# Kernel tuning notes

Measured on AMD Instinct MI355X. Metric: run time of the kernel, lower is better.

## Reference

```python
import jax, jax.numpy as jnp
import numpy as np

B, T, C = 2, 2048, 1024
N_HEAD = 16
HEAD_DIM = C // N_HEAD


def setup_inputs() -> dict:
    key = jax.random.key(0)
    ks = jax.random.split(key, 5)
    s = 0.02
    return {
        "x": jax.random.normal(ks[0], (B, T, C), dtype=jnp.float32),
        "W_kqv": jax.random.normal(ks[1], (C, 3 * C), dtype=jnp.float32) * s,
        "b_kqv": jax.random.normal(ks[2], (3 * C,), dtype=jnp.float32) * s,
        "W_proj": jax.random.normal(ks[3], (C, C), dtype=jnp.float32) * s,
        "b_proj": jax.random.normal(ks[4], (C,), dtype=jnp.float32) * s,
    }


def reference(x, W_kqv, b_kqv, W_proj, b_proj):
    Bx, Tx, Cx = x.shape
    qkv = x @ W_kqv + b_kqv                      # [B, T, 3C]
    q, k, v = jnp.split(qkv, 3, axis=-1)
    # [B, H, T, D]
    q = q.reshape(Bx, Tx, N_HEAD, HEAD_DIM).transpose(0, 2, 1, 3)
    k = k.reshape(Bx, Tx, N_HEAD, HEAD_DIM).transpose(0, 2, 1, 3)
    v = v.reshape(Bx, Tx, N_HEAD, HEAD_DIM).transpose(0, 2, 1, 3)
    scale = 1.0 / jnp.sqrt(jnp.asarray(HEAD_DIM, dtype=x.dtype))
    att = jnp.einsum("bhqd,bhkd->bhqk", q, k) * scale  # [B, H, T, T]
    causal = jnp.tril(jnp.ones((Tx, Tx), dtype=bool))   # [T, T]
    att = jnp.where(causal[None, None], att, jnp.float32(-jnp.inf))
    att = jax.nn.softmax(att, axis=-1)
    y = jnp.einsum("bhqk,bhkd->bhqd", att, v)            # [B, H, T, D]
    y = y.transpose(0, 2, 1, 3).reshape(Bx, Tx, Cx)
    out = y @ W_proj + b_proj
    return out, k, v
```

## Files before the change

kernel.cpp:

```cpp
#include <hip/hip_runtime.h>


#define DEVI __device__ __forceinline__

typedef unsigned short ushort_t;
typedef unsigned long long u64_t;
typedef __attribute__((ext_vector_type(4))) unsigned short us4;
typedef __attribute__((ext_vector_type(8))) unsigned short ushort8;
typedef __attribute__((ext_vector_type(4))) float f32x4;
typedef __attribute__((ext_vector_type(8))) __bf16 bf16x8;

DEVI unsigned short f2bf(float f) {
  union { float f; unsigned int u; } c; c.f = f;
  unsigned int u = c.u;
  unsigned int r = (u + 0x7FFFu + ((u >> 16) & 1u)) >> 16;
  return (unsigned short)r;
}

DEVI float exp2v(float x) {
  float r;
  asm("v_exp_f32 %0, %1\n\ts_nop 0" : "=v"(r) : "v"(x));
  return r;
}

DEVI unsigned int cvtpk(float lo, float hi) {
  unsigned int r;
  asm("v_cvt_pk_bf16_f32 %0, %1, %2" : "=v"(r) : "v"(lo), "v"(hi));
  return r;
}

DEVI f32x4 mfma16(ushort8 a, ushort8 b, f32x4 c) {
  return __builtin_amdgcn_mfma_f32_16x16x32_bf16(
      __builtin_bit_cast(bf16x8, a), __builtin_bit_cast(bf16x8, b), c, 0, 0, 0);
}

typedef const __attribute__((address_space(1))) void* gptr_t;
typedef __attribute__((address_space(3))) void* lptr_t;
#define GLOAD_LDS16(g, l) \
  __builtin_amdgcn_global_load_lds((gptr_t)(g), (lptr_t)(l), 16, 0, 0)

DEVI void bar() {
  asm volatile("" ::: "memory");
  __builtin_amdgcn_s_barrier();
  asm volatile("" ::: "memory");
}
#define VMCNT(n) asm volatile("s_waitcnt vmcnt(" #n ")" ::: "memory")


__global__ void cast_x_kernel(const float* __restrict__ in,
                              ushort_t* __restrict__ out, int n8) {
  int i = blockIdx.x * blockDim.x + threadIdx.x;
  if (i >= n8) return;
  const f32x4* p = (const f32x4*)in;
  f32x4 a = p[2 * i], b = p[2 * i + 1];
  ushort8 o;
  o[0] = f2bf(a[0]); o[1] = f2bf(a[1]); o[2] = f2bf(a[2]); o[3] = f2bf(a[3]);
  o[4] = f2bf(b[0]); o[5] = f2bf(b[1]); o[6] = f2bf(b[2]); o[7] = f2bf(b[3]);
  ((ushort8*)out)[i] = o;
}

__global__ void transpose_cast_kernel(const float* __restrict__ in,
                                      ushort_t* __restrict__ out, int R, int Cin) {
  __shared__ float tile[32][33];
  int c0 = blockIdx.x * 32, r0 = blockIdx.y * 32;
  int tx = threadIdx.x & 31, ty = threadIdx.x >> 5;
#pragma unroll
  for (int it = 0; it < 4; ++it)
    tile[ty + it * 8][tx] = in[(size_t)(r0 + ty + it * 8) * Cin + c0 + tx];
  __syncthreads();
#pragma unroll
  for (int it = 0; it < 4; ++it)
    out[(size_t)(c0 + ty + it * 8) * R + r0 + tx] = f2bf(tile[tx][ty + it * 8]);
}


__global__ __launch_bounds__(256) void gemm_bt_kernel(
    const ushort_t* __restrict__ A, const ushort_t* __restrict__ Bt,
    const float* __restrict__ bias, float* __restrict__ outF,
    float* __restrict__ outK, float* __restrict__ outV,
    ushort_t* __restrict__ Qb, ushort_t* __restrict__ Kb, ushort_t* __restrict__ Vb,
    int M, int N, int K, int mode) {
  __shared__ __align__(16) ushort_t As[128 * 64];
  __shared__ __align__(16) ushort_t Bs[128 * 64];
  const int tid = threadIdx.x;
  const int w = tid >> 6, lane = tid & 63;
  const int wr = w >> 1, wc = w & 1;
  const int nbx = gridDim.x;
  const int nwg = nbx * gridDim.y;
  const int orig = blockIdx.x + nbx * blockIdx.y;
  const int tile = (orig & 7) * (nwg >> 3) + (orig >> 3);
  const int bx = tile % nbx, by = tile / nbx;
  const int m0 = by * 128, n0 = bx * 128;
  const int l15 = lane & 15, lhi = lane >> 4;
  const int rowA = lane >> 3;
  const int sgc = (((lane & 7) ^ ((lane >> 3) & 7)) << 3);

  f32x4 acc[4][4] = {};

  const int nk = K >> 6;
  for (int kt = 0; kt < nk; ++kt) {
    const size_t k0 = (size_t)kt << 6;
    if (kt) bar();
#pragma unroll
    for (int it = 0; it < 4; ++it) {
      const int rbase = (w * 4 + it) * 8;
      GLOAD_LDS16(A + (size_t)(m0 + rbase + rowA) * K + k0 + sgc, &As[rbase * 64]);
      GLOAD_LDS16(Bt + (size_t)(n0 + rbase + rowA) * K + k0 + sgc, &Bs[rbase * 64]);
    }
    VMCNT(0);
    bar();
#pragma unroll
    for (int kk = 0; kk < 2; ++kk) {
      const int gof = (((kk * 4 + lhi) ^ (l15 & 7)) << 3);
      ushort8 a[4], b[4];
#pragma unroll
      for (int i = 0; i < 4; ++i)
        a[i] = *(const ushort8*)&As[(wr * 64 + i * 16 + l15) * 64 + gof];
#pragma unroll
      for (int j = 0; j < 4; ++j)
        b[j] = *(const ushort8*)&Bs[(wc * 64 + j * 16 + l15) * 64 + gof];
#pragma unroll
      for (int i = 0; i < 4; ++i)
#pragma unroll
        for (int j = 0; j < 4; ++j) acc[i][j] = mfma16(a[i], b[j], acc[i][j]);
    }
  }

  const float QSCALE = 0.18033688011112042f;
#pragma unroll
  for (int i = 0; i < 4; ++i) {
#pragma unroll
    for (int j = 0; j < 4; ++j) {
      const int nn = n0 + wc * 64 + j * 16 + l15;
      const float bv = bias[nn];
#pragma unroll
      for (int r = 0; r < 4; ++r) {
        const int mm = m0 + wr * 64 + i * 16 + lhi * 4 + r;
        const float v = acc[i][j][r] + bv;
        if (mode == 0) {
          outF[(size_t)mm * N + nn] = v;
        } else {
          const int bb = mm >> 11, t = mm & 2047;
          const int c = nn & 1023, h = c >> 6, d = c & 63;
          const size_t idx = ((size_t)(bb * 16 + h) * 2048 + t) * 64 + d;
          const int sec = nn >> 10;
          if (sec == 0) {
            Qb[idx] = f2bf(v * QSCALE);
          } else if (sec == 1) {
            outK[idx] = v; Kb[idx] = f2bf(v);
          } else {
            outV[idx] = v; Vb[idx] = f2bf(v);
          }
        }
      }
    }
  }
}


__global__ __launch_bounds__(256) void attn_kernel(
    const ushort_t* __restrict__ Qb, const ushort_t* __restrict__ Kb,
    const ushort_t* __restrict__ Vb, ushort_t* __restrict__ Yb) {
  __shared__ __align__(16) ushort_t Ks[2][64 * 64];
  __shared__ __align__(16) ushort_t Vt[2][64 * 72];
  __shared__ __align__(16) ushort_t Pl[4 * 16 * 72];
  const int id = blockIdx.x;
  const int xcd = id & 7, win = id >> 3;
  const int qt = 31 - (win >> 2);
  const int bh = xcd + 8 * (win & 3);
  const int b = bh >> 4, h = bh & 15;
  const int tid = threadIdx.x, w = tid >> 6, lane = tid & 63;
  const int l15 = lane & 15, lhi = lane >> 4;
  const int swzP = 2 * (l15 & 3);
  const size_t base = (size_t)bh * 2048 * 64;
  const float NEG_INF = -__builtin_inff();
  ushort_t* myP = &Pl[w * 16 * 72];

  const int vd0 = (tid & 15) * 4;
  const int vt0b = (tid >> 4) * 2;

  const int nkt = qt + 1;

  ushort8 qf[2];
  {
    const size_t qrow = base + (size_t)(qt * 64 + w * 16 + l15) * 64;
    qf[0] = *(const ushort8*)&Qb[qrow + lhi * 8];
    qf[1] = *(const ushort8*)&Qb[qrow + 32 + lhi * 8];
  }
  float m_s = NEG_INF, l_s = 0.f;
  f32x4 o[4] = {};

  {
#pragma unroll
    for (int it = 0; it < 2; ++it) {
      const int chunk = tid + it * 256;
      const int row = chunk >> 3, g = chunk & 7;
      const int sg = g ^ (row & 7);
      GLOAD_LDS16(Kb + base + (size_t)row * 64 + sg * 8, &Ks[0][chunk * 8]);
    }
#pragma unroll
    for (int it = 0; it < 2; ++it) {
      const int t0 = vt0b + it * 32;
      const ushort_t* vp = Vb + base + (size_t)t0 * 64 + vd0;
      u64_t a = *(const u64_t*)vp;
      u64_t c = *(const u64_t*)(vp + 64);
      us4 av = __builtin_bit_cast(us4, a);
      us4 cv = __builtin_bit_cast(us4, c);
#pragma unroll
      for (int i = 0; i < 4; ++i) {
        const int d = vd0 + i;
        const int scg = (t0 >> 3) ^ ((d >> 3) & 7);
        unsigned int wv = (unsigned int)av[i] | ((unsigned int)cv[i] << 16);
        *(unsigned int*)&Vt[0][d * 72 + scg * 8 + (t0 & 7)] = wv;
      }
    }
  }
  __syncthreads();

  for (int kt = 0; kt < nkt; ++kt) {
    const int cur = kt & 1, nxt = cur ^ 1;
    const bool pf = (kt + 1 < nkt);
    u64_t va[2], vc[2];
    if (pf) {
      const size_t tb = base + (size_t)(kt + 1) * 64 * 64;
#pragma unroll
      for (int it = 0; it < 2; ++it) {
        const int chunk = tid + it * 256;
        const int row = chunk >> 3, g = chunk & 7;
        const int sg = g ^ (row & 7);
        GLOAD_LDS16(Kb + tb + (size_t)row * 64 + sg * 8, &Ks[nxt][chunk * 8]);
      }
#pragma unroll
      for (int it = 0; it < 2; ++it) {
        const int t0 = vt0b + it * 32;
        const ushort_t* vp = Vb + tb + (size_t)t0 * 64 + vd0;
        va[it] = *(const u64_t*)vp;
        vc[it] = *(const u64_t*)(vp + 64);
      }
    }

    f32x4 s[4] = {};
#pragma unroll
    for (int kk = 0; kk < 2; ++kk) {
#pragma unroll
      for (int j = 0; j < 4; ++j) {
        const int g = (kk * 4 + lhi) ^ (l15 & 7);
        ushort8 kb = *(const ushort8*)&Ks[cur][(j * 16 + l15) * 64 + g * 8];
        s[j] = mfma16(kb, qf[kk], s[j]);
      }
    }
    const int qloc = w * 16 + l15;
    if (kt == qt) {
#pragma unroll
      for (int j = 0; j < 4; ++j)
#pragma unroll
        for (int r = 0; r < 4; ++r)
          if ((j * 16 + lhi * 4 + r) > qloc) s[j][r] = NEG_INF;
    }

    float pmax = s[0][0];
#pragma unroll
    for (int j = 0; j < 4; ++j)
#pragma unroll
      for (int r = 0; r < 4; ++r) pmax = fmaxf(pmax, s[j][r]);
    pmax = fmaxf(pmax, __shfl_xor(pmax, 16));
    pmax = fmaxf(pmax, __shfl_xor(pmax, 32));
    if (__any(pmax - m_s > 8.0f)) {
      const float mnew = fmaxf(m_s, pmax);
      const float al = exp2v(m_s - mnew);
      m_s = mnew;
      l_s *= al;
#pragma unroll
      for (int df = 0; df < 4; ++df)
#pragma unroll
        for (int r = 0; r < 4; ++r) o[df][r] *= al;
    }
    float rsum = 0.f;
#pragma unroll
    for (int j = 0; j < 4; ++j)
#pragma unroll
      for (int r = 0; r < 4; ++r) {
        const float pe = exp2v(s[j][r] - m_s);
        s[j][r] = pe;
        rsum += pe;
      }
    rsum += __shfl_xor(rsum, 16);
    rsum += __shfl_xor(rsum, 32);
    l_s += rsum;

#pragma unroll
    for (int j = 0; j < 4; ++j) {
      const unsigned int w0 = cvtpk(s[j][0], s[j][1]);
      const unsigned int w1 = cvtpk(s[j][2], s[j][3]);
      const u64_t dw = (u64_t)w0 | ((u64_t)w1 << 32);
      const int cg = j * 2 + (lhi >> 1);
      *(u64_t*)&myP[l15 * 72 + ((cg ^ swzP) << 3) + ((lhi & 1) << 2)] = dw;
    }

#pragma unroll
    for (int kk = 0; kk < 2; ++kk) {
      ushort8 pa = *(const ushort8*)&myP[l15 * 72 + (((kk * 4 + lhi) ^ swzP) << 3)];
#pragma unroll
      for (int df = 0; df < 4; ++df) {
        const int r = df * 16 + l15;
        const int g = (kk * 4 + lhi) ^ ((r >> 3) & 7);
        ushort8 vb = *(const ushort8*)&Vt[cur][r * 72 + g * 8];
        o[df] = mfma16(vb, pa, o[df]);
      }
    }

    if (pf) {
#pragma unroll
      for (int it = 0; it < 2; ++it) {
        const int t0 = vt0b + it * 32;
        us4 av = __builtin_bit_cast(us4, va[it]);
        us4 cv = __builtin_bit_cast(us4, vc[it]);
#pragma unroll
        for (int i = 0; i < 4; ++i) {
          const int d = vd0 + i;
          const int scg = (t0 >> 3) ^ ((d >> 3) & 7);
          unsigned int wv = (unsigned int)av[i] | ((unsigned int)cv[i] << 16);
          *(unsigned int*)&Vt[nxt][d * 72 + scg * 8 + (t0 & 7)] = wv;
        }
      }
    }
    __syncthreads();
  }

  const float inv = 1.0f / l_s;
  const size_t yrow = (size_t)(b * 2048 + qt * 64 + w * 16 + l15) * 1024 + h * 64;
#pragma unroll
  for (int df = 0; df < 4; ++df) {
    us4 ov;
#pragma unroll
    for (int r = 0; r < 4; ++r) ov[r] = f2bf(o[df][r] * inv);
    *(us4*)&Yb[yrow + df * 16 + lhi * 4] = ov;
  }
}


extern "C" void kernel_launch(void* const* d_in, const int* in_sizes, int n_in,
                              void* d_out, int out_size, void* d_ws, size_t ws_size,
                              hipStream_t stream) {
  const float* x      = (const float*)d_in[0];
  const float* W_kqv  = (const float*)d_in[1];
  const float* b_kqv  = (const float*)d_in[2];
  const float* W_proj = (const float*)d_in[3];
  const float* b_proj = (const float*)d_in[4];
  float* out  = (float*)d_out;
  float* outK = out + 4194304;
  float* outV = out + 8388608;

  char* ws = (char*)d_ws;
  ushort_t* Xb  = (ushort_t*)(ws);
  ushort_t* Wkt = (ushort_t*)(ws + ((size_t)8 << 20));
  ushort_t* Wpt = (ushort_t*)(ws + ((size_t)14 << 20));
  ushort_t* Qb  = (ushort_t*)(ws + ((size_t)16 << 20));
  ushort_t* Kb  = (ushort_t*)(ws + ((size_t)24 << 20));
  ushort_t* Vb  = (ushort_t*)(ws + ((size_t)32 << 20));
  ushort_t* Yb  = Xb;

  cast_x_kernel<<<2048, 256, 0, stream>>>(x, Xb, 524288);
  transpose_cast_kernel<<<dim3(96, 32), 256, 0, stream>>>(W_kqv, Wkt, 1024, 3072);
  transpose_cast_kernel<<<dim3(32, 32), 256, 0, stream>>>(W_proj, Wpt, 1024, 1024);
  gemm_bt_kernel<<<dim3(24, 32), 256, 0, stream>>>(
      Xb, Wkt, b_kqv, nullptr, outK, outV, Qb, Kb, Vb, 4096, 3072, 1024, 1);
  attn_kernel<<<1024, 256, 0, stream>>>(Qb, Kb, Vb, Yb);
  gemm_bt_kernel<<<dim3(8, 32), 256, 0, stream>>>(
      Yb, Wpt, b_proj, out, nullptr, nullptr, nullptr, nullptr, nullptr,
      4096, 1024, 1024, 0);
}
```

Before: 117.8 us.

## Load K fragments straight to registers with double-buffered prefetch, drop K LDS

K tiles are no longer staged through shared memory. Each lane loads its MFMA K fragments directly from global memory into two register sets that alternate each step, and the loop is unrolled by two so the buffers swap statically. LDS address offsets are precomputed outside the loop, and the max and sum reductions use trees instead of serial chains. This removes the K LDS traffic and the LDS footprint it needed, at the cost of 64 extra VGPRs for K fragments, which risks occupancy loss and spills, plus redundant global loads of K across the four waves.

```diff
diff --git a/kernel.cpp b/kernel.cpp
--- a/kernel.cpp
+++ b/kernel.cpp
@@ -161,7 +161,6 @@
 __global__ __launch_bounds__(256) void attn_kernel(
     const ushort_t* __restrict__ Qb, const ushort_t* __restrict__ Kb,
     const ushort_t* __restrict__ Vb, ushort_t* __restrict__ Yb) {
-  __shared__ __align__(16) ushort_t Ks[2][64 * 64];
   __shared__ __align__(16) ushort_t Vt[2][64 * 72];
   __shared__ __align__(16) ushort_t Pl[4 * 16 * 72];
   const int id = blockIdx.x;
@@ -175,11 +174,44 @@
   const size_t base = (size_t)bh * 2048 * 64;
   const float NEG_INF = -__builtin_inff();
   ushort_t* myP = &Pl[w * 16 * 72];
-
+  const int nkt = qt + 1;
+
+  int kgo[8];
+#pragma unroll
+  for (int kk = 0; kk < 2; ++kk)
+#pragma unroll
+    for (int j = 0; j < 4; ++j)
+      kgo[kk * 4 + j] = (j * 16 + l15) * 64 + kk * 32 + lhi * 8;
   const int vd0 = (tid & 15) * 4;
   const int vt0b = (tid >> 4) * 2;
-
-  const int nkt = qt + 1;
+  const int vgo0 = vt0b * 64 + vd0;
+  const int vgo1 = (vt0b + 32) * 64 + vd0;
+  int lvo[2][4];
+#pragma unroll
+  for (int it = 0; it < 2; ++it) {
+    const int t0 = vt0b + it * 32;
+#pragma unroll
+    for (int i = 0; i < 4; ++i) {
+      const int d = vd0 + i;
+      const int scg = (t0 >> 3) ^ ((d >> 3) & 7);
+      lvo[it][i] = d * 72 + scg * 8 + (t0 & 7);
+    }
+  }
+  int pwo[4], pro[2];
+#pragma unroll
+  for (int j = 0; j < 4; ++j)
+    pwo[j] = l15 * 72 + (((j * 2 + (lhi >> 1)) ^ swzP) << 3) + ((lhi & 1) << 2);
+#pragma unroll
+  for (int kk = 0; kk < 2; ++kk)
+    pro[kk] = l15 * 72 + (((kk * 4 + lhi) ^ swzP) << 3);
+  int vro[8];
+#pragma unroll
+  for (int kk = 0; kk < 2; ++kk)
+#pragma unroll
+    for (int df = 0; df < 4; ++df) {
+      const int r = df * 16 + l15;
+      vro[kk * 4 + df] = r * 72 + (((kk * 4 + lhi) ^ ((r >> 3) & 7)) << 3);
+    }
 
   ushort8 qf[2];
   {
@@ -189,67 +221,53 @@
   }
   float m_s = NEG_INF, l_s = 0.f;
   f32x4 o[4] = {};
+  ushort8 kfA[8], kfB[8];
 
   {
 #pragma unroll
-    for (int it = 0; it < 2; ++it) {
-      const int chunk = tid + it * 256;
-      const int row = chunk >> 3, g = chunk & 7;
-      const int sg = g ^ (row & 7);
-      GLOAD_LDS16(Kb + base + (size_t)row * 64 + sg * 8, &Ks[0][chunk * 8]);
-    }
-#pragma unroll
-    for (int it = 0; it < 2; ++it) {
-      const int t0 = vt0b + it * 32;
-      const ushort_t* vp = Vb + base + (size_t)t0 * 64 + vd0;
-      u64_t a = *(const u64_t*)vp;
-      u64_t c = *(const u64_t*)(vp + 64);
-      us4 av = __builtin_bit_cast(us4, a);
-      us4 cv = __builtin_bit_cast(us4, c);
-#pragma unroll
-      for (int i = 0; i < 4; ++i) {
-        const int d = vd0 + i;
-        const int scg = (t0 >> 3) ^ ((d >> 3) & 7);
-        unsigned int wv = (unsigned int)av[i] | ((unsigned int)cv[i] << 16);
-        *(unsigned int*)&Vt[0][d * 72 + scg * 8 + (t0 & 7)] = wv;
-      }
+    for (int i = 0; i < 8; ++i)
+      kfA[i] = *(const ushort8*)&Kb[base + kgo[i]];
+    const ushort_t* vp0 = Vb + base + vgo0;
+    const ushort_t* vp1 = Vb + base + vgo1;
+    u64_t a0 = *(const u64_t*)vp0, c0 = *(const u64_t*)(vp0 + 64);
+    u64_t a1 = *(const u64_t*)vp1, c1 = *(const u64_t*)(vp1 + 64);
+    us4 av0 = __builtin_bit_cast(us4, a0), cv0 = __builtin_bit_cast(us4, c0);
+    us4 av1 = __builtin_bit_cast(us4, a1), cv1 = __builtin_bit_cast(us4, c1);
+#pragma unroll
+    for (int i = 0; i < 4; ++i) {
+      *(unsigned int*)&Vt[0][lvo[0][i]] =
+          (unsigned int)av0[i] | ((unsigned int)cv0[i] << 16);
+      *(unsigned int*)&Vt[0][lvo[1][i]] =
+          (unsigned int)av1[i] | ((unsigned int)cv1[i] << 16);
     }
   }
   __syncthreads();
 
-  for (int kt = 0; kt < nkt; ++kt) {
-    const int cur = kt & 1, nxt = cur ^ 1;
+  const int qloc = w * 16 + l15;
+
+  auto step = [&](int kt, ushort8 (&kfu)[8], ushort8 (&kfl)[8],
+                  const int cur) __attribute__((always_inline)) {
+    const int nxt = cur ^ 1;
     const bool pf = (kt + 1 < nkt);
-    u64_t va[2], vc[2];
+    const size_t tb = base + (size_t)(kt + 1) * 4096;
+    u64_t va0 = 0, vc0 = 0, va1 = 0, vc1 = 0;
     if (pf) {
-      const size_t tb = base + (size_t)(kt + 1) * 64 * 64;
-#pragma unroll
-      for (int it = 0; it < 2; ++it) {
-        const int chunk = tid + it * 256;
-        const int row = chunk >> 3, g = chunk & 7;
-        const int sg = g ^ (row & 7);
-        GLOAD_LDS16(Kb + tb + (size_t)row * 64 + sg * 8, &Ks[nxt][chunk * 8]);
-      }
-#pragma unroll
-      for (int it = 0; it < 2; ++it) {
-        const int t0 = vt0b + it * 32;
-        const ushort_t* vp = Vb + tb + (size_t)t0 * 64 + vd0;
-        va[it] = *(const u64_t*)vp;
-        vc[it] = *(const u64_t*)(vp + 64);
-      }
+      const ushort_t* vp0 = Vb + tb + vgo0;
+      const ushort_t* vp1 = Vb + tb + vgo1;
+      va0 = *(const u64_t*)vp0; vc0 = *(const u64_t*)(vp0 + 64);
+      va1 = *(const u64_t*)vp1; vc1 = *(const u64_t*)(vp1 + 64);
+#pragma unroll
+      for (int i = 0; i < 8; ++i)
+        kfl[i] = *(const ushort8*)&Kb[tb + kgo[i]];
     }
 
     f32x4 s[4] = {};
 #pragma unroll
-    for (int kk = 0; kk < 2; ++kk) {
-#pragma unroll
-      for (int j = 0; j < 4; ++j) {
-        const int g = (kk * 4 + lhi) ^ (l15 & 7);
-        ushort8 kb = *(const ushort8*)&Ks[cur][(j * 16 + l15) * 64 + g * 8];
-        s[j] = mfma16(kb, qf[kk], s[j]);
-      }
-    }
-    const int qloc = w * 16 + l15;
+    for (int kk = 0; kk < 2; ++kk)
+#pragma unroll
+      for (int j = 0; j < 4; ++j)
+        s[j] = mfma16(kfu[kk * 4 + j], qf[kk], s[j]);
+
     if (kt == qt) {
 #pragma unroll
       for (int j = 0; j < 4; ++j)
@@ -258,11 +276,11 @@
           if ((j * 16 + lhi * 4 + r) > qloc) s[j][r] = NEG_INF;
     }
 
-    float pmax = s[0][0];
+    float mj[4];
 #pragma unroll
     for (int j = 0; j < 4; ++j)
-#pragma unroll
-      for (int r = 0; r < 4; ++r) pmax = fmaxf(pmax, s[j][r]);
+      mj[j] = fmaxf(fmaxf(s[j][0], s[j][1]), fmaxf(s[j][2], s[j][3]));
+    float pmax = fmaxf(fmaxf(mj[0], mj[1]), fmaxf(mj[2], mj[3]));
     pmax = fmaxf(pmax, __shfl_xor(pmax, 16));
     pmax = fmaxf(pmax, __shfl_xor(pmax, 32));
     if (__any(pmax - m_s > 8.0f)) {
@@ -275,15 +293,15 @@
 #pragma unroll
         for (int r = 0; r < 4; ++r) o[df][r] *= al;
     }
-    float rsum = 0.f;
 #pragma unroll
     for (int j = 0; j < 4; ++j)
 #pragma unroll
-      for (int r = 0; r < 4; ++r) {
-        const float pe = exp2v(s[j][r] - m_s);
-        s[j][r] = pe;
-        rsum += pe;
-      }
+      for (int r = 0; r < 4; ++r) s[j][r] = exp2v(s[j][r] - m_s);
+    float rj[4];
+#pragma unroll
+    for (int j = 0; j < 4; ++j)
+      rj[j] = (s[j][0] + s[j][1]) + (s[j][2] + s[j][3]);
+    float rsum = (rj[0] + rj[1]) + (rj[2] + rj[3]);
     rsum += __shfl_xor(rsum, 16);
     rsum += __shfl_xor(rsum, 32);
     l_s += rsum;
@@ -292,39 +310,39 @@
     for (int j = 0; j < 4; ++j) {
       const unsigned int w0 = cvtpk(s[j][0], s[j][1]);
       const unsigned int w1 = cvtpk(s[j][2], s[j][3]);
-      const u64_t dw = (u64_t)w0 | ((u64_t)w1 << 32);
-      const int cg = j * 2 + (lhi >> 1);
-      *(u64_t*)&myP[l15 * 72 + ((cg ^ swzP) << 3) + ((lhi & 1) << 2)] = dw;
+      *(u64_t*)&myP[pwo[j]] = (u64_t)w0 | ((u64_t)w1 << 32);
     }
 
 #pragma unroll
     for (int kk = 0; kk < 2; ++kk) {
-      ushort8 pa = *(const ushort8*)&myP[l15 * 72 + (((kk * 4 + lhi) ^ swzP) << 3)];
+      ushort8 pa = *(const ushort8*)&myP[pro[kk]];
 #pragma unroll
       for (int df = 0; df < 4; ++df) {
-        const int r = df * 16 + l15;
-        const int g = (kk * 4 + lhi) ^ ((r >> 3) & 7);
-        ushort8 vb = *(const ushort8*)&Vt[cur][r * 72 + g * 8];
+        ushort8 vb = *(const ushort8*)&Vt[cur][vro[kk * 4 + df]];
         o[df] = mfma16(vb, pa, o[df]);
       }
     }
 
     if (pf) {
-#pragma unroll
-      for (int it = 0; it < 2; ++it) {
-        const int t0 = vt0b + it * 32;
-        us4 av = __builtin_bit_cast(us4, va[it]);
-        us4 cv = __builtin_bit_cast(us4, vc[it]);
-#pragma unroll
-        for (int i = 0; i < 4; ++i) {
-          const int d = vd0 + i;
-          const int scg = (t0 >> 3) ^ ((d >> 3) & 7);
-          unsigned int wv = (unsigned int)av[i] | ((unsigned int)cv[i] << 16);
-          *(unsigned int*)&Vt[nxt][d * 72 + scg * 8 + (t0 & 7)] = wv;
-        }
+      us4 av0 = __builtin_bit_cast(us4, va0), cv0 = __builtin_bit_cast(us4, vc0);
+      us4 av1 = __builtin_bit_cast(us4, va1), cv1 = __builtin_bit_cast(us4, vc1);
+#pragma unroll
+      for (int i = 0; i < 4; ++i) {
+        *(unsigned int*)&Vt[nxt][lvo[0][i]] =
+            (unsigned int)av0[i] | ((unsigned int)cv0[i] << 16);
+        *(unsigned int*)&Vt[nxt][lvo[1][i]] =
+            (unsigned int)av1[i] | ((unsigned int)cv1[i] << 16);
       }
     }
     __syncthreads();
+  };
+
+  int kt = 0;
+  for (;;) {
+    step(kt, kfA, kfB, 0);
+    if (++kt == nkt) break;
+    step(kt, kfB, kfA, 1);
+    if (++kt == nkt) break;
   }
 
   const float inv = 1.0f / l_s;
```

Measured after the change: 147.9 us. 1.26x slower.
